# Kernel tuning notes

Measured on AMD Instinct MI355X. Metric: run time of the kernel, lower is better.

Reference implementation:

```python
import jax, jax.numpy as jnp
import numpy as np

ATTN_SCALE = 0.12
HEAD_DIM = 128


def _rms_norm(x):
    # F.rms_norm with no weight; eps defaults to machine eps of dtype
    eps = jnp.asarray(jnp.finfo(x.dtype).eps, x.dtype)
    return x * jax.lax.rsqrt(jnp.mean(x * x, axis=-1, keepdims=True) + eps)


def _rope(x):
    # x: [B, T, H, D]; standard rotary over (first-half, second-half) pairs
    T, D = x.shape[1], x.shape[-1]
    half = D // 2
    inv_freq = 1.0 / (10000.0 ** (jnp.arange(half, dtype=jnp.float32) / half))
    ang = jnp.arange(T, dtype=jnp.float32)[:, None] * inv_freq[None, :]  # [T, half]
    cos = jnp.cos(ang)[None, :, None, :].astype(x.dtype)
    sin = jnp.sin(ang)[None, :, None, :].astype(x.dtype)
    x1, x2 = x[..., :half], x[..., half:]
    return jnp.concatenate([x1 * cos - x2 * sin, x1 * sin + x2 * cos], axis=-1)


def setup_inputs() -> dict:
    key = jax.random.key(0)
    ks = jax.random.split(key, 4)
    B, T, dim, H, hd = 4, 2048, 1024, 8, HEAD_DIM
    hdim = H * hd
    std = 0.5 * dim ** (-0.5)
    bound = (3.0 ** 0.5) * std
    return {
        "x": jax.random.normal(ks[0], (B, T, dim), jnp.float32),
        "ve": jax.random.normal(ks[1], (B, T, hdim), jnp.float32),
        "qkv_w": jax.random.uniform(ks[2], (3, hdim, dim), jnp.float32, -bound, bound),
        "lambdas": jnp.array([0.5, 0.5], jnp.float32),
        "c_proj_w": jax.random.normal(ks[3], (dim, hdim), jnp.float32) * (hdim ** -0.5),
        "c_proj_b": jnp.zeros((dim,), jnp.float32),
    }


def reference(x, ve, qkv_w, lambdas, c_proj_w, c_proj_b):
    B, T, dim = x.shape
    hdim = qkv_w.shape[1]
    hd = HEAD_DIM
    H = hdim // hd
    # fused QKV projection: [B,T,3,H,hd]
    qkv = jnp.einsum('btd,ehd->bteh', x, qkv_w.reshape(3 * hdim, dim).reshape(3 * H, hd, dim).reshape(3 * hdim // hd, hd, dim))
    qkv = jnp.einsum('btd,fd->btf', x, qkv_w.reshape(3 * hdim, dim)).reshape(B, T, 3, H, hd)
    q, k, v = qkv[:, :, 0], qkv[:, :, 1], qkv[:, :, 2]  # each [B,T,H,hd]
    q, k = _rms_norm(q), _rms_norm(k)
    q, k = _rope(q), _rope(k)
    v = lambdas[0] * v + lambdas[1] * ve.reshape(B, T, H, hd)
    # causal SDPA with custom scale
    scores = jnp.einsum('bthd,bshd->bhts', q, k) * ATTN_SCALE  # [B,H,T,T]
    causal = jnp.tril(jnp.ones((T, T), dtype=bool))
    scores = jnp.where(causal[None, None], scores, jnp.finfo(scores.dtype).min)
    p = jax.nn.softmax(scores, axis=-1)
    y = jnp.einsum('bhts,bshd->bthd', p, v).reshape(B, T, hdim)
    return y @ c_proj_w.T + c_proj_b
```

## Files before the change

### kernel.cpp

```cpp
#include <hip/hip_runtime.h>
#include <math.h>

typedef unsigned short u16;
typedef short bf16x8 __attribute__((ext_vector_type(8)));
typedef u16 u16x2 __attribute__((ext_vector_type(2)));
typedef u16 u16x4 __attribute__((ext_vector_type(4)));
typedef u16 u16x8 __attribute__((ext_vector_type(8)));
typedef float f32x2 __attribute__((ext_vector_type(2)));
typedef float f32x4 __attribute__((ext_vector_type(4)));
typedef float f32x16 __attribute__((ext_vector_type(16)));

typedef __attribute__((address_space(1))) const void gvoid_t;
typedef __attribute__((address_space(3))) void lvoid_t;

__device__ __forceinline__ u16 f2bf(float f) {
  union { float f; unsigned u; } v; v.f = f;
  unsigned r = v.u + 0x7fffu + ((v.u >> 16) & 1u);
  return (u16)(r >> 16);
}
__device__ __forceinline__ float bf2f(u16 h) {
  union { unsigned u; float f; } v; v.u = ((unsigned)h) << 16;
  return v.f;
}
__device__ __forceinline__ f32x4 mfma16(bf16x8 a, bf16x8 b, f32x4 c) {
  return __builtin_amdgcn_mfma_f32_16x16x32_bf16(a, b, c, 0, 0, 0);
}
__device__ __forceinline__ f32x16 mfma32(bf16x8 a, bf16x8 b, f32x16 c) {
  return __builtin_amdgcn_mfma_f32_32x32x16_bf16(a, b, c, 0, 0, 0);
}
__device__ __forceinline__ void gload_lds16(const void* g, void* l) {
  __builtin_amdgcn_global_load_lds((gvoid_t*)g, (lvoid_t*)l, 16, 0, 0);
}
__device__ __forceinline__ unsigned cvtpk_bf16(float lo, float hi) {
  unsigned r;
  asm("v_cvt_pk_bf16_f32 %0, %1, %2" : "=v"(r) : "v"(lo), "v"(hi));
  return r;
}
__device__ __forceinline__ void pswap32(unsigned& a, unsigned& b) {
  asm("v_permlane32_swap_b32 %0, %1" : "+v"(a), "+v"(b));
}

#if __has_builtin(__builtin_amdgcn_exp2f)
#define EXPW(x) __builtin_amdgcn_exp2f(x)
#define SCALE_W 0.17312354f
#define DEFER_THR 11.5415603f
#else
#define EXPW(x) __expf(x)
#define SCALE_W 0.12f
#define DEFER_THR 8.0f
#endif

#define BAR() __builtin_amdgcn_s_barrier()
#define WAITLGKM()                          \
  asm volatile("s_waitcnt lgkmcnt(0)");     \
  __builtin_amdgcn_sched_barrier(0)
#define WAITVMC(N)                                    \
  do {                                                \
    __builtin_amdgcn_s_waitcnt(0x0F70 | (N));         \
    __builtin_amdgcn_sched_barrier(0);                \
  } while (0)

__global__ __launch_bounds__(256) void cvt_bf16_kernel(const float* __restrict__ in,
                                                       u16* __restrict__ out, int n4) {
  int i = blockIdx.x * 256 + threadIdx.x;
  if (i >= n4) return;
  f32x4 v = *(const f32x4*)(in + (size_t)i * 4);
  u16x4 o;
  o[0] = f2bf(v[0]); o[1] = f2bf(v[1]); o[2] = f2bf(v[2]); o[3] = f2bf(v[3]);
  *(u16x4*)(out + (size_t)i * 4) = o;
}

__global__ __launch_bounds__(256) void rope_tab_kernel(float* __restrict__ ct,
                                                       float* __restrict__ st) {
  int i = blockIdx.x * 256 + threadIdx.x;
  int t = i >> 6, j = i & 63;
  float inv = powf(10000.f, -(float)j * (1.0f / 64.0f));
  float ang = (float)t * inv;
  ct[i] = cosf(ang);
  st[i] = sinf(ang);
}

template <int BM, int OUTF32>
__global__ __launch_bounds__(512, 1) void gemm2ph_kernel(
    const u16* __restrict__ A, const u16* __restrict__ B, void* __restrict__ C,
    const float* __restrict__ bias, int M, int N, int K, int nbn) {
  constexpr int AH = BM / 2;
  constexpr int WR = AH / 2;
  constexpr int MI = WR / 16;
  constexpr int NACC = 2 * MI;
  constexpr int AROUNDS = AH / 64;
  constexpr int SA = AROUNDS;
  constexpr int SB = 2;
  __shared__ u16 Alds[2][BM * 64];
  __shared__ u16 Blds[2][256 * 64];
  int nwg = gridDim.x;
  int cpx = nwg >> 3;
  int bid = blockIdx.x;
  int swz = (bid & 7) * cpx + (bid >> 3);
  int bm = (swz & 3) + 4 * (swz / (4 * nbn));
  int bn = (swz >> 2) % nbn;
  size_t m0 = (size_t)bm * BM, n0 = (size_t)bn * 256;
  int tid = threadIdx.x, wid = tid >> 6, lane = tid & 63;
  int wr = wid >> 2, wc = wid & 3, l15 = lane & 15, l4 = lane >> 4;
  int srow = tid >> 3, sch = tid & 7;

  const u16* Abase = A + m0 * K;
  const u16* Bbase = B + n0 * K;

  f32x4 acc[NACC][4];
#pragma unroll
  for (int m = 0; m < NACC; m++)
#pragma unroll
    for (int n = 0; n < 4; n++) acc[m][n] = f32x4{0.f, 0.f, 0.f, 0.f};

  auto stageA = [&](int buf, int kt, int half) {
#pragma unroll
    for (int r = 0; r < AROUNDS; ++r) {
      int row = AH * half + 64 * r + srow;
      gload_lds16(Abase + (size_t)row * K + kt * 64 + 8 * (sch ^ (row & 7)),
                  &Alds[buf][(AH * half + 64 * r + 8 * wid) * 64]);
    }
  };
  auto stageB = [&](int buf, int kt, int half) {
#pragma unroll
    for (int r = 0; r < 2; ++r) {
      int row = 128 * half + 64 * r + srow;
      gload_lds16(Bbase + (size_t)row * K + kt * 64 + 8 * (sch ^ (row & 7)),
                  &Blds[buf][(128 * half + 64 * r + 8 * wid) * 64]);
    }
  };
  auto rdA = [&](int buf, int half, bf16x8 (&a)[MI][2]) {
#pragma unroll
    for (int mi = 0; mi < MI; ++mi)
#pragma unroll
      for (int kk = 0; kk < 2; ++kk) {
        int row = AH * half + WR * wr + 16 * mi + l15;
        a[mi][kk] = *(const bf16x8*)((const char*)(&Alds[buf][0]) + row * 128 +
                                     ((kk * 64 + 16 * l4) ^ ((row & 7) << 4)));
      }
  };
  auto rdB = [&](int buf, int half, bf16x8 (&bb)[2][2]) {
#pragma unroll
    for (int ni = 0; ni < 2; ++ni)
#pragma unroll
      for (int kk = 0; kk < 2; ++kk) {
        int row = 64 * wc + 32 * half + 16 * ni + l15;
        bb[ni][kk] = *(const bf16x8*)((const char*)(&Blds[buf][0]) + row * 128 +
                                      ((kk * 64 + 16 * l4) ^ ((row & 7) << 4)));
      }
  };

#define QUAD(AF, BF, MH, NH)                                              \
  do {                                                                    \
    _Pragma("unroll") for (int mi = 0; mi < MI; ++mi)                     \
        _Pragma("unroll") for (int ni = 0; ni < 2; ++ni)                  \
            _Pragma("unroll") for (int kk = 0; kk < 2; ++kk)              \
                acc[MI * MH + mi][2 * NH + ni] =                          \
        mfma16(AF[mi][kk], BF[ni][kk], acc[MI * MH + mi][2 * NH + ni]);   \
  } while (0)

  stageB(0, 0, 0);
  stageB(0, 0, 1);
  stageA(0, 0, 0);
  stageA(0, 0, 1);
  WAITVMC(SA);
  BAR();

  int nk = K >> 6;
  bf16x8 a0[MI][2], a1[MI][2], b0[2][2], b1[2][2];
  for (int t = 0; t < nk; ++t) {
    int buf = t & 1, nxt = buf ^ 1;
    bool pf = (t + 1 < nk);
    rdA(buf, 0, a0);
    rdB(buf, 0, b0);
    rdB(buf, 1, b1);
    if (pf) { stageB(nxt, t + 1, 0); stageB(nxt, t + 1, 1); stageA(nxt, t + 1, 0); }
    BAR();
    WAITLGKM();
    __builtin_amdgcn_s_setprio(1);
    QUAD(a0, b0, 0, 0);
    QUAD(a0, b1, 0, 1);
    __builtin_amdgcn_s_setprio(0);
    if (pf) { WAITVMC(2 * SB + SA); } else { WAITVMC(0); }
    BAR();
    rdA(buf, 1, a1);
    if (pf) stageA(nxt, t + 1, 1);
    BAR();
    WAITLGKM();
    __builtin_amdgcn_s_setprio(1);
    QUAD(a1, b0, 1, 0);
    QUAD(a1, b1, 1, 1);
    __builtin_amdgcn_s_setprio(0);
    if (pf) { WAITVMC(SA); } else { WAITVMC(0); }
    BAR();
  }

#pragma unroll
  for (int mi = 0; mi < NACC; ++mi) {
#pragma unroll
    for (int ni = 0; ni < 4; ++ni) {
      size_t row = m0 + AH * (mi / MI) + WR * wr + 16 * (mi % MI) + 4 * l4;
      size_t col = n0 + 64 * wc + 16 * ni + l15;
#pragma unroll
      for (int i = 0; i < 4; ++i) {
        float v = acc[mi][ni][i];
        if constexpr (OUTF32) {
          ((float*)C)[(row + i) * N + col] = v + bias[col];
        } else {
          ((u16*)C)[(row + i) * N + col] = f2bf(v);
        }
      }
    }
  }
#undef QUAD
}

__global__ __launch_bounds__(256) void transform_kernel(
    const u16* __restrict__ qkv, const float* __restrict__ ve,
    const float* __restrict__ lam, const float* __restrict__ ct,
    const float* __restrict__ st, u16* __restrict__ qn, u16* __restrict__ kn,
    u16* __restrict__ vt) {
  constexpr int T = 2048;
  __shared__ u16 vtile[64][136];
  int tt = blockIdx.x, bh = blockIdx.y;
  int b = bh >> 3, h = bh & 7;
  int tid = threadIdx.x, wid = tid >> 6, lane = tid & 63;
  int lsub = lane & 15, lrow = lane >> 4;
  float l0 = lam[0], l1 = lam[1];
  int d0 = 8 * lsub;
  float sgn = (lsub < 8) ? -1.f : 1.f;
  int jj = d0 & 63;
#pragma unroll
  for (int it = 0; it < 4; ++it) {
    int tl = wid * 16 + it * 4 + lrow;
    int t = tt * 64 + tl;
    size_t base = ((size_t)(b * T + t)) * 3072 + h * 128 + d0;
    u16x8 qraw = *(const u16x8*)(qkv + base);
    u16x8 kraw = *(const u16x8*)(qkv + base + 1024);
    u16x8 vraw = *(const u16x8*)(qkv + base + 2048);
    const float* vep = ve + ((size_t)(b * T + t)) * 1024 + h * 128 + d0;
    f32x4 ve0 = *(const f32x4*)(vep);
    f32x4 ve1 = *(const f32x4*)(vep + 4);
    float q[8], k[8];
    float sq = 0.f, sk = 0.f;
#pragma unroll
    for (int i = 0; i < 8; ++i) {
      q[i] = bf2f(qraw[i]); k[i] = bf2f(kraw[i]);
      sq += q[i] * q[i]; sk += k[i] * k[i];
    }
#pragma unroll
    for (int m = 1; m < 16; m <<= 1) {
      sq += __shfl_xor(sq, m);
      sk += __shfl_xor(sk, m);
    }
    float qs = rsqrtf(sq * (1.f / 128.f) + 1.1920929e-7f);
    float ks = rsqrtf(sk * (1.f / 128.f) + 1.1920929e-7f);
#pragma unroll
    for (int i = 0; i < 8; ++i) { q[i] *= qs; k[i] *= ks; }
    f32x4 c0 = *(const f32x4*)(ct + t * 64 + jj);
    f32x4 c1 = *(const f32x4*)(ct + t * 64 + jj + 4);
    f32x4 s0 = *(const f32x4*)(st + t * 64 + jj);
    f32x4 s1 = *(const f32x4*)(st + t * 64 + jj + 4);
    u16x8 oq, ok, ov;
#pragma unroll
    for (int i = 0; i < 8; ++i) {
      float qp = __shfl_xor(q[i], 8), kp = __shfl_xor(k[i], 8);
      float cc = (i < 4) ? c0[i & 3] : c1[i & 3];
      float ss = (i < 4) ? s0[i & 3] : s1[i & 3];
      oq[i] = f2bf(q[i] * cc + sgn * qp * ss);
      ok[i] = f2bf(k[i] * cc + sgn * kp * ss);
      float vv = (i < 4) ? ve0[i & 3] : ve1[i & 3];
      ov[i] = f2bf(l0 * bf2f(vraw[i]) + l1 * vv);
    }
    size_t orow = ((size_t)bh * T + t) * 128 + d0;
    *(u16x8*)(qn + orow) = oq;
    *(u16x8*)(kn + orow) = ok;
    *(u16x8*)&vtile[tl][d0] = ov;
  }
  __syncthreads();
#pragma unroll
  for (int it = 0; it < 4; ++it) {
    int ci = it * 256 + tid;
    int d = ci >> 3, c8 = ci & 7;
    u16x8 o;
#pragma unroll
    for (int u = 0; u < 8; u++) o[u] = vtile[c8 * 8 + u][d];
    *(u16x8*)(vt + ((size_t)bh * 128 + d) * T + tt * 64 + c8 * 8) = o;
  }
}

__global__ __launch_bounds__(256, 2) void attn_kernel(
    const u16* __restrict__ Qn, const u16* __restrict__ Kn,
    const u16* __restrict__ Vt, u16* __restrict__ Y) {
  constexpr int T = 2048;
  __shared__ u16 Klds[2][64 * 128];
  __shared__ u16 Vlds[2][128 * 64];
  int bid = blockIdx.x;
  int g = bid >> 5;
  int s = (g < 8) ? (15 - g) : (g - 8);
  int bh = bid & 31;
  int b = bh >> 3, h = bh & 7;
  int tid = threadIdx.x, wid = tid >> 6, lane = tid & 63;
  int l31 = lane & 31, hh = lane >> 5;
  const u16* Qb = Qn + (size_t)bh * T * 128;
  const u16* Kb = Kn + (size_t)bh * T * 128;
  const u16* Vb = Vt + (size_t)bh * 128 * T;
  int q0w = s * 128 + wid * 32;
  int qmaxw = q0w + 31;
  int ktend = 2 * s + 2;
  int qg = q0w + l31;

  bf16x8 qf[8];
  {
    const u16* qr = Qb + (size_t)(q0w + l31) * 128 + 8 * hh;
#pragma unroll
    for (int ks = 0; ks < 8; ks++) qf[ks] = *(const bf16x8*)(qr + 16 * ks);
  }
  f32x16 acc[4];
#pragma unroll
  for (int mt = 0; mt < 4; mt++)
#pragma unroll
    for (int r = 0; r < 16; r++) acc[mt][r] = 0.f;
  float m_run = -1e30f, l_run = 0.f;

  auto stage = [&](int buf, int kt) {
#pragma unroll
    for (int it = 0; it < 4; ++it) {
      int id = wid * 256 + it * 64 + lane;
      int r = id >> 4, c = id & 15;
      gload_lds16(Kb + (size_t)(kt * 64 + r) * 128 + 8 * (c ^ (r & 7)),
                  &Klds[buf][(size_t)(wid * 256 + it * 64) * 8]);
      int rv = id >> 3, cv = id & 7;
      gload_lds16(Vb + (size_t)rv * T + kt * 64 + 8 * (cv ^ (rv & 7)),
                  &Vlds[buf][(size_t)(wid * 256 + it * 64) * 8]);
    }
  };

  stage(0, 0);

  for (int kt = 0; kt < ktend; ++kt) {
    int cur = kt & 1;
    if (kt + 1 < ktend) {
      stage(cur ^ 1, kt + 1);
      WAITVMC(8);
    } else {
      WAITVMC(0);
    }
    BAR();
    if (kt * 64 <= qmaxw) {
      const char* kb = (const char*)&Klds[cur][0];
      const char* vb = (const char*)&Vlds[cur][0];
      int rswz = (l31 & 7) << 4;
      f32x16 st0, st1;
#pragma unroll
      for (int r = 0; r < 16; r++) { st0[r] = 0.f; st1[r] = 0.f; }
      __builtin_amdgcn_s_setprio(1);
#pragma unroll
      for (int ks = 0; ks < 8; ks++) {
        bf16x8 kf0 = *(const bf16x8*)(kb + ((l31 * 256 + 32 * ks + 16 * hh) ^ rswz));
        bf16x8 kf1 = *(const bf16x8*)(kb + (((32 + l31) * 256 + 32 * ks + 16 * hh) ^ rswz));
        st0 = mfma32(kf0, qf[ks], st0);
        st1 = mfma32(kf1, qf[ks], st1);
      }
      __builtin_amdgcn_s_setprio(0);
      bool edge = (kt == (qmaxw >> 6));
      if (edge) {
#pragma unroll
        for (int r = 0; r < 16; r++) {
          int kvb = kt * 64 + (r & 3) + 8 * (r >> 2) + 4 * hh;
          if (kvb > qg) st0[r] = -1e30f;
          if (kvb + 32 > qg) st1[r] = -1e30f;
        }
      }
      float m8[8];
#pragma unroll
      for (int r = 0; r < 8; r++)
        m8[r] = fmaxf(fmaxf(st0[r], st0[r + 8]), fmaxf(st1[r], st1[r + 8]));
#pragma unroll
      for (int r = 0; r < 4; r++) m8[r] = fmaxf(m8[r], m8[r + 4]);
      float pm = fmaxf(fmaxf(m8[0], m8[1]), fmaxf(m8[2], m8[3]));
      pm = fmaxf(pm, __shfl_xor(pm, 32));
      float pmn = pm * SCALE_W;
      bool nos = __all(pmn <= m_run + DEFER_THR);
      float mnew = nos ? m_run : fmaxf(m_run, pmn);
      if (!nos) {
        float alpha = EXPW(m_run - mnew);
        l_run *= alpha;
#pragma unroll
        for (int mt = 0; mt < 4; mt++)
#pragma unroll
          for (int r = 0; r < 16; r++) acc[mt][r] *= alpha;
        m_run = mnew;
      }
      float sa = 0.f, sb = 0.f, sc = 0.f, sd = 0.f;
#pragma unroll
      for (int r = 0; r < 4; r++) {
        st0[r]      = EXPW(fmaf(st0[r],      SCALE_W, -mnew)); sa += st0[r];
        st0[r + 4]  = EXPW(fmaf(st0[r + 4],  SCALE_W, -mnew)); sb += st0[r + 4];
        st0[r + 8]  = EXPW(fmaf(st0[r + 8],  SCALE_W, -mnew)); sc += st0[r + 8];
        st0[r + 12] = EXPW(fmaf(st0[r + 12], SCALE_W, -mnew)); sd += st0[r + 12];
        st1[r]      = EXPW(fmaf(st1[r],      SCALE_W, -mnew)); sa += st1[r];
        st1[r + 4]  = EXPW(fmaf(st1[r + 4],  SCALE_W, -mnew)); sb += st1[r + 4];
        st1[r + 8]  = EXPW(fmaf(st1[r + 8],  SCALE_W, -mnew)); sc += st1[r + 8];
        st1[r + 12] = EXPW(fmaf(st1[r + 12], SCALE_W, -mnew)); sd += st1[r + 12];
      }
      float ps = (sa + sb) + (sc + sd);
      ps += __shfl_xor(ps, 32);
      l_run += ps;
      unsigned pA0[4], pB0[4], pA1[4], pB1[4];
#pragma unroll
      for (int rr = 0; rr < 4; rr++) {
        pA0[rr] = cvtpk_bf16(st0[4 * rr], st0[4 * rr + 1]);
        pB0[rr] = cvtpk_bf16(st0[4 * rr + 2], st0[4 * rr + 3]);
        pA1[rr] = cvtpk_bf16(st1[4 * rr], st1[4 * rr + 1]);
        pB1[rr] = cvtpk_bf16(st1[4 * rr + 2], st1[4 * rr + 3]);
      }
      bf16x8 pf[4];
#pragma unroll
      for (int ks2 = 0; ks2 < 4; ks2++) {
        int k1 = ks2 & 1;
        unsigned a0, b0, a1, b1;
        if (ks2 < 2) { a0 = pA0[2 * k1]; b0 = pA0[2 * k1 + 1]; a1 = pB0[2 * k1]; b1 = pB0[2 * k1 + 1]; }
        else         { a0 = pA1[2 * k1]; b0 = pA1[2 * k1 + 1]; a1 = pB1[2 * k1]; b1 = pB1[2 * k1 + 1]; }
        pswap32(a0, b0);
        pswap32(a1, b1);
        union { unsigned w[4]; bf16x8 v; } u;
        u.w[0] = a0; u.w[1] = a1; u.w[2] = b0; u.w[3] = b1;
        pf[ks2] = u.v;
      }
      __builtin_amdgcn_s_setprio(1);
#pragma unroll
      for (int mt = 0; mt < 4; mt++) {
        int row = 32 * mt + l31;
#pragma unroll
        for (int ks2 = 0; ks2 < 4; ks2++) {
          bf16x8 vf = *(const bf16x8*)(vb + ((row * 128 + 32 * ks2 + 16 * hh) ^ rswz));
          acc[mt] = mfma32(vf, pf[ks2], acc[mt]);
        }
      }
      __builtin_amdgcn_s_setprio(0);
    }
    BAR();
  }
  float linv = 1.f / l_run;
  size_t yrow = (size_t)b * T + q0w + l31;
  u16* yp = Y + yrow * 1024 + h * 128;
#pragma unroll
  for (int mt = 0; mt < 4; mt++) {
#pragma unroll
    for (int rr = 0; rr < 4; rr++) {
      u16x4 o;
#pragma unroll
      for (int i = 0; i < 4; i++) o[i] = f2bf(acc[mt][4 * rr + i] * linv);
      *(u16x4*)(yp + 32 * mt + 8 * rr + 4 * hh) = o;
    }
  }
}

extern "C" void kernel_launch(void* const* d_in, const int* in_sizes, int n_in,
                              void* d_out, int out_size, void* d_ws, size_t ws_size,
                              hipStream_t stream) {
  (void)in_sizes; (void)n_in; (void)out_size; (void)ws_size;
  const float* x = (const float*)d_in[0];
  const float* ve = (const float*)d_in[1];
  const float* qkvw = (const float*)d_in[2];
  const float* lam = (const float*)d_in[3];
  const float* cpw = (const float*)d_in[4];
  const float* cpb = (const float*)d_in[5];
  float* out = (float*)d_out;
  char* ws = (char*)d_ws;

  u16* xb   = (u16*)(ws + 0);
  u16* wqkv = (u16*)(ws + 16777216);
  u16* wp   = (u16*)(ws + 23068672);
  u16* qkv  = (u16*)(ws + 25165824);
  u16* qn   = (u16*)(ws + 75497472);
  u16* kn   = (u16*)(ws + 92274688);
  u16* vt   = (u16*)(ws + 109051904);
  float* ctab = (float*)(ws + 125829120);
  float* stab = (float*)(ws + 126353408);
  u16* y = xb;

  rope_tab_kernel<<<512, 256, 0, stream>>>(ctab, stab);
  cvt_bf16_kernel<<<8192, 256, 0, stream>>>(x, xb, 2097152);
  cvt_bf16_kernel<<<3072, 256, 0, stream>>>(qkvw, wqkv, 786432);
  cvt_bf16_kernel<<<1024, 256, 0, stream>>>(cpw, wp, 262144);
  gemm2ph_kernel<256, 0><<<384, 512, 0, stream>>>(xb, wqkv, qkv, nullptr, 8192, 3072, 1024, 12);
  transform_kernel<<<dim3(32, 32), 256, 0, stream>>>(qkv, ve, lam, ctab, stab, qn, kn, vt);
  attn_kernel<<<512, 256, 0, stream>>>(qn, kn, vt, y);
  gemm2ph_kernel<128, 1><<<256, 512, 0, stream>>>(y, wp, out, cpb, 8192, 1024, 1024, 4);
}
```

Measured before the change: 202.2 us.

## Restructure GEMM main loop into four-phase MFMA/prefetch schedule with contiguous warp tiles

Replaces the two-phase GEMM loop with a four-phase schedule. Each phase loads one quarter of the A/B fragments, issues a slice of the next tile's global-to-LDS prefetch, and runs one quadrant of MFMAs. Warp row tiles become contiguous (WM = BM/2 per warp row) instead of split across two A halves. Fewer fragment registers are live at once, and prefetch is spread more evenly across the iteration. The cost is more barriers per k-step and a full WAITVMC(0) at the end of each iteration, which may expose load latency.

```diff
diff --git a/kernel.cpp b/kernel.cpp
--- a/kernel.cpp
+++ b/kernel.cpp
@@ -81,16 +81,13 @@
 }
 
 template <int BM, int OUTF32>
-__global__ __launch_bounds__(512, 1) void gemm2ph_kernel(
+__global__ __launch_bounds__(512, 1) void gemm4p_kernel(
     const u16* __restrict__ A, const u16* __restrict__ B, void* __restrict__ C,
     const float* __restrict__ bias, int M, int N, int K, int nbn) {
-  constexpr int AH = BM / 2;
-  constexpr int WR = AH / 2;
-  constexpr int MI = WR / 16;
+  constexpr int WM = BM / 2;
+  constexpr int MI = WM / 32;
   constexpr int NACC = 2 * MI;
-  constexpr int AROUNDS = AH / 64;
-  constexpr int SA = AROUNDS;
-  constexpr int SB = 2;
+  constexpr int AR = BM / 64;
   __shared__ u16 Alds[2][BM * 64];
   __shared__ u16 Blds[2][256 * 64];
   int nwg = gridDim.x;
@@ -113,85 +110,90 @@
 #pragma unroll
     for (int n = 0; n < 4; n++) acc[m][n] = f32x4{0.f, 0.f, 0.f, 0.f};
 
-  auto stageA = [&](int buf, int kt, int half) {
-#pragma unroll
-    for (int r = 0; r < AROUNDS; ++r) {
-      int row = AH * half + 64 * r + srow;
+  auto stageR = [&](int buf, int kt, int r) {
+    if (r < AR) {
+      int row = 64 * r + srow;
       gload_lds16(Abase + (size_t)row * K + kt * 64 + 8 * (sch ^ (row & 7)),
-                  &Alds[buf][(AH * half + 64 * r + 8 * wid) * 64]);
+                  &Alds[buf][(64 * r + 8 * wid) * 64]);
+    } else {
+      int row = 64 * (r - AR) + srow;
+      gload_lds16(Bbase + (size_t)row * K + kt * 64 + 8 * (sch ^ (row & 7)),
+                  &Blds[buf][(64 * (r - AR) + 8 * wid) * 64]);
     }
   };
-  auto stageB = [&](int buf, int kt, int half) {
-#pragma unroll
-    for (int r = 0; r < 2; ++r) {
-      int row = 128 * half + 64 * r + srow;
-      gload_lds16(Bbase + (size_t)row * K + kt * 64 + 8 * (sch ^ (row & 7)),
-                  &Blds[buf][(128 * half + 64 * r + 8 * wid) * 64]);
-    }
-  };
-  auto rdA = [&](int buf, int half, bf16x8 (&a)[MI][2]) {
+  auto rdA = [&](int buf, int qm, bf16x8 (&a)[MI][2]) {
 #pragma unroll
     for (int mi = 0; mi < MI; ++mi)
 #pragma unroll
       for (int kk = 0; kk < 2; ++kk) {
-        int row = AH * half + WR * wr + 16 * mi + l15;
+        int row = WM * wr + (WM / 2) * qm + 16 * mi + l15;
         a[mi][kk] = *(const bf16x8*)((const char*)(&Alds[buf][0]) + row * 128 +
                                      ((kk * 64 + 16 * l4) ^ ((row & 7) << 4)));
       }
   };
-  auto rdB = [&](int buf, int half, bf16x8 (&bb)[2][2]) {
+  auto rdB = [&](int buf, int qn, bf16x8 (&bb)[2][2]) {
 #pragma unroll
     for (int ni = 0; ni < 2; ++ni)
 #pragma unroll
       for (int kk = 0; kk < 2; ++kk) {
-        int row = 64 * wc + 32 * half + 16 * ni + l15;
+        int row = 64 * wc + 32 * qn + 16 * ni + l15;
         bb[ni][kk] = *(const bf16x8*)((const char*)(&Blds[buf][0]) + row * 128 +
                                       ((kk * 64 + 16 * l4) ^ ((row & 7) << 4)));
       }
   };
 
-#define QUAD(AF, BF, MH, NH)                                              \
+#define QUADX(AF, BF, QM, QN)                                             \
   do {                                                                    \
+    __builtin_amdgcn_s_setprio(1);                                        \
     _Pragma("unroll") for (int mi = 0; mi < MI; ++mi)                     \
         _Pragma("unroll") for (int ni = 0; ni < 2; ++ni)                  \
             _Pragma("unroll") for (int kk = 0; kk < 2; ++kk)              \
-                acc[MI * MH + mi][2 * NH + ni] =                          \
-        mfma16(AF[mi][kk], BF[ni][kk], acc[MI * MH + mi][2 * NH + ni]);   \
+                acc[MI * QM + mi][2 * QN + ni] =                          \
+        mfma16(AF[mi][kk], BF[ni][kk], acc[MI * QM + mi][2 * QN + ni]);   \
+    __builtin_amdgcn_s_setprio(0);                                        \
   } while (0)
 
-  stageB(0, 0, 0);
-  stageB(0, 0, 1);
-  stageA(0, 0, 0);
-  stageA(0, 0, 1);
-  WAITVMC(SA);
+  constexpr int NR = AR + 4;
+#pragma unroll
+  for (int r = 0; r < NR; ++r) stageR(0, 0, r);
+  WAITVMC(0);
   BAR();
 
   int nk = K >> 6;
-  bf16x8 a0[MI][2], a1[MI][2], b0[2][2], b1[2][2];
+  bf16x8 a[MI][2], b0[2][2], b1[2][2];
   for (int t = 0; t < nk; ++t) {
     int buf = t & 1, nxt = buf ^ 1;
     bool pf = (t + 1 < nk);
-    rdA(buf, 0, a0);
+    rdA(buf, 0, a);
     rdB(buf, 0, b0);
+    if (pf) {
+      if constexpr (BM == 256) { stageR(nxt, t + 1, 0); stageR(nxt, t + 1, 1); stageR(nxt, t + 1, 2); }
+      else { stageR(nxt, t + 1, 0); stageR(nxt, t + 1, 1); }
+    }
+    BAR();
+    WAITLGKM();
+    QUADX(a, b0, 0, 0);
+    BAR();
     rdB(buf, 1, b1);
-    if (pf) { stageB(nxt, t + 1, 0); stageB(nxt, t + 1, 1); stageA(nxt, t + 1, 0); }
+    if (pf) {
+      if constexpr (BM == 256) { stageR(nxt, t + 1, 3); stageR(nxt, t + 1, 4); stageR(nxt, t + 1, 5); }
+      else { stageR(nxt, t + 1, 2); stageR(nxt, t + 1, 3); }
+    }
     BAR();
     WAITLGKM();
-    __builtin_amdgcn_s_setprio(1);
-    QUAD(a0, b0, 0, 0);
-    QUAD(a0, b1, 0, 1);
-    __builtin_amdgcn_s_setprio(0);
-    if (pf) { WAITVMC(2 * SB + SA); } else { WAITVMC(0); }
-    BAR();
-    rdA(buf, 1, a1);
-    if (pf) stageA(nxt, t + 1, 1);
+    QUADX(a, b1, 0, 1);
+    BAR();
+    rdA(buf, 1, a);
+    if (pf) {
+      if constexpr (BM == 256) { stageR(nxt, t + 1, 6); stageR(nxt, t + 1, 7); }
+      else { stageR(nxt, t + 1, 4); stageR(nxt, t + 1, 5); }
+    }
     BAR();
     WAITLGKM();
-    __builtin_amdgcn_s_setprio(1);
-    QUAD(a1, b0, 1, 0);
-    QUAD(a1, b1, 1, 1);
-    __builtin_amdgcn_s_setprio(0);
-    if (pf) { WAITVMC(SA); } else { WAITVMC(0); }
+    QUADX(a, b0, 1, 0);
+    BAR();
+    QUADX(a, b1, 1, 1);
+    WAITVMC(0);
     BAR();
   }
 
@@ -199,7 +201,7 @@
   for (int mi = 0; mi < NACC; ++mi) {
 #pragma unroll
     for (int ni = 0; ni < 4; ++ni) {
-      size_t row = m0 + AH * (mi / MI) + WR * wr + 16 * (mi % MI) + 4 * l4;
+      size_t row = m0 + WM * wr + 16 * mi + 4 * l4;
       size_t col = n0 + 64 * wc + 16 * ni + l15;
 #pragma unroll
       for (int i = 0; i < 4; ++i) {
@@ -212,7 +214,7 @@
       }
     }
   }
-#undef QUAD
+#undef QUADX
 }
 
 __global__ __launch_bounds__(256) void transform_kernel(
@@ -485,8 +487,8 @@
   cvt_bf16_kernel<<<8192, 256, 0, stream>>>(x, xb, 2097152);
   cvt_bf16_kernel<<<3072, 256, 0, stream>>>(qkvw, wqkv, 786432);
   cvt_bf16_kernel<<<1024, 256, 0, stream>>>(cpw, wp, 262144);
-  gemm2ph_kernel<256, 0><<<384, 512, 0, stream>>>(xb, wqkv, qkv, nullptr, 8192, 3072, 1024, 12);
+  gemm4p_kernel<256, 0><<<384, 512, 0, stream>>>(xb, wqkv, qkv, nullptr, 8192, 3072, 1024, 12);
   transform_kernel<<<dim3(32, 32), 256, 0, stream>>>(qkv, ve, lam, ctab, stab, qn, kn, vt);
   attn_kernel<<<512, 256, 0, stream>>>(qn, kn, vt, y);
-  gemm2ph_kernel<128, 1><<<256, 512, 0, stream>>>(y, wp, out, cpb, 8192, 1024, 1024, 4);
-}
+  gemm4p_kernel<128, 1><<<256, 512, 0, stream>>>(y, wp, out, cpb, 8192, 1024, 1024, 4);
+}
```

New measurement: 199.3 us. Within noise of the previous version (-1.4%).
